# Kernel tuning notes

Hardware: AMD Instinct MI355X
Metric: run time of the kernel (lower is better)

## Reference

```python
import jax, jax.numpy as jnp
import numpy as np

N_NODES = 50000
N_EDGES = 800000
IN_CH = 64
OUT_CH = 64
PRIOR_VAR = 1.0


def setup_inputs() -> dict:
    key = jax.random.key(0)
    ks = jax.random.split(key, 10)
    mean = jax.random.normal(ks[0], (N_NODES, IN_CH), dtype=jnp.float32)
    std = jax.random.uniform(ks[1], (N_NODES, IN_CH), dtype=jnp.float32)
    edge_index = jax.random.randint(ks[2], (2, N_EDGES), 0, N_NODES, dtype=jnp.int32)
    edge_weight = jax.random.uniform(ks[3], (N_EDGES,), dtype=jnp.float32)
    # Bayesian GCN parameters (xavier-ish mu, log_sigma init -3.0) for mean- and std-branches
    scale = float(np.sqrt(6.0 / (IN_CH + OUT_CH)))
    mu_mean = jax.random.uniform(ks[4], (IN_CH, OUT_CH), minval=-scale, maxval=scale, dtype=jnp.float32)
    log_sigma_mean = jnp.full((IN_CH, OUT_CH), -3.0, dtype=jnp.float32)
    mu_std = jax.random.uniform(ks[5], (IN_CH, OUT_CH), minval=-scale, maxval=scale, dtype=jnp.float32)
    log_sigma_std = jnp.full((IN_CH, OUT_CH), -3.0, dtype=jnp.float32)
    # reparameterization noise (drawn once so reference is deterministic)
    eps_mean = jax.random.normal(ks[6], (IN_CH, OUT_CH), dtype=jnp.float32)
    eps_std = jax.random.normal(ks[7], (IN_CH, OUT_CH), dtype=jnp.float32)
    return {
        "mean": mean, "std": std, "edge_index": edge_index, "edge_weight": edge_weight,
        "mu_mean": mu_mean, "log_sigma_mean": log_sigma_mean, "eps_mean": eps_mean,
        "mu_std": mu_std, "log_sigma_std": log_sigma_std, "eps_std": eps_std,
    }


def _gcn_propagate(x, weight, edge_index, edge_weight):
    # support = x @ W; then gather src rows, scale by edge_weight, scatter-add to dst
    support = jnp.matmul(x, weight)                      # [N, out]
    src, dst = edge_index[0], edge_index[1]
    msg = edge_weight[:, None] * support[src]            # [E, out]
    return jax.ops.segment_sum(msg, dst, num_segments=N_NODES)


def _kl(mu, log_sigma):
    pv = PRIOR_VAR
    kl = 0.5 * (jnp.exp(2.0 * log_sigma) / pv + mu ** 2 / pv
                - 2.0 * log_sigma - jnp.log(jnp.asarray(pv, mu.dtype)) - 1.0)
    return kl.sum()


def reference(mean, std, edge_index, edge_weight,
              mu_mean, log_sigma_mean, eps_mean,
              mu_std, log_sigma_std, eps_std):
    # mean branch
    w_mean = mu_mean + eps_mean * jnp.exp(log_sigma_mean)
    new_mean = _gcn_propagate(mean, w_mean, edge_index, edge_weight)
    kl_mean = _kl(mu_mean, log_sigma_mean)
    # std branch operates on variance with squared edge weights
    var = std ** 2
    w_std = mu_std + eps_std * jnp.exp(log_sigma_std)
    new_log_var = _gcn_propagate(var, w_std, edge_index, edge_weight ** 2)
    kl_std = _kl(mu_std, log_sigma_std)
    new_std = jnp.sqrt(jnp.exp(new_log_var) + 1e-6)
    total_kl = kl_mean + kl_std
    return (new_mean, new_std, total_kl)
```

## Files before the change

kernel.cpp:

```cpp
#include <hip/hip_runtime.h>

#define N_NODES 50000
#define N_EDGES 800000
#define CH 64
#define OUT_OFF_STD (N_NODES * CH)
#define OUT_OFF_KL  (2 * N_NODES * CH)
#define CAP 64

#define NGRP 8
#define NPG 6250
#define FILL_CHUNK 2048
#define FILL_CHUNKS 391
#define FILL_BLOCKS (NGRP * FILL_CHUNKS)
#define GEMM_BLOCKS 782
#define GATHER_CHUNKS 1563

typedef __attribute__((ext_vector_type(8))) short short8;
typedef __attribute__((ext_vector_type(4))) float f32x4;

__device__ __forceinline__ int rl_i(unsigned v, int lane) {
    return __builtin_amdgcn_readlane((int)v, lane);
}
__device__ __forceinline__ unsigned f2bf(float f) {
    unsigned u = __float_as_uint(f);
    return (u + 0x7fffu + ((u >> 16) & 1u)) >> 16;
}

__global__ __launch_bounds__(256) void wkl_kernel(
    const float* __restrict__ mu_m, const float* __restrict__ ls_m,
    const float* __restrict__ eps_m,
    const float* __restrict__ mu_s, const float* __restrict__ ls_s,
    const float* __restrict__ eps_s,
    unsigned short* __restrict__ fragBm, unsigned short* __restrict__ fragBv,
    float* __restrict__ kl_out)
{
    __shared__ unsigned short Wm[CH * CH];
    __shared__ unsigned short Wv[CH * CH];
    float kl = 0.0f;
    for (int i = threadIdx.x; i < CH * CH; i += 256) {
        float mu = mu_m[i], ls = ls_m[i];
        Wm[i] = (unsigned short)f2bf(mu + eps_m[i] * expf(ls));
        kl += 0.5f * (expf(2.0f * ls) + mu * mu - 2.0f * ls - 1.0f);
        mu = mu_s[i]; ls = ls_s[i];
        Wv[i] = (unsigned short)f2bf(mu + eps_s[i] * expf(ls));
        kl += 0.5f * (expf(2.0f * ls) + mu * mu - 2.0f * ls - 1.0f);
    }
    __syncthreads();
    for (int f = threadIdx.x; f < CH * CH; f += 256) {
        int j = f & 7, l = (f >> 3) & 63, ch = f >> 9;
        int k = (ch & 1) * 32 + ((l >> 4) & 3) * 8 + j;
        int n = (ch >> 1) * 16 + (l & 15);
        fragBm[f] = Wm[k * CH + n];
        fragBv[f] = Wv[k * CH + n];
    }
    for (int off = 32; off > 0; off >>= 1)
        kl += __shfl_down(kl, off, 64);
    __shared__ float red[4];
    if ((threadIdx.x & 63) == 0) red[threadIdx.x >> 6] = kl;
    __syncthreads();
    if (threadIdx.x == 0)
        kl_out[0] = red[0] + red[1] + red[2] + red[3];
}

__global__ __launch_bounds__(256) void gemfill_kernel(
    const float* __restrict__ mean, const float* __restrict__ stdv,
    const unsigned short* __restrict__ fragBm,
    const unsigned short* __restrict__ fragBv,
    const int* __restrict__ ei, const float* __restrict__ ew,
    int* __restrict__ cur, uint2* __restrict__ bins,
    unsigned* __restrict__ sup)
{
    const int tid = threadIdx.x;

    if (blockIdx.x < FILL_BLOCKS) {
        const int g = blockIdx.x & (NGRP - 1);
        const int chunk = blockIdx.x >> 3;
        const int base = chunk * FILL_CHUNK;
        const int lo = g * NPG;
#pragma unroll
        for (int r = 0; r < FILL_CHUNK / 256; ++r) {
            int e = base + r * 256 + tid;
            if (e < N_EDGES) {
                int dst = ei[N_EDGES + e];
                if ((unsigned)(dst - lo) < (unsigned)NPG) {
                    int src = ei[e];
                    float w = ew[e];
                    int slot = atomicAdd(&cur[dst], 1);
                    if (slot < CAP)
                        bins[(size_t)dst * CAP + slot] =
                            make_uint2((unsigned)src, __float_as_uint(w));
                }
            }
        }
        return;
    }

    const int lane = tid & 63, wave = tid >> 6;
    const int row0 = (blockIdx.x - FILL_BLOCKS) * 64 + wave * 16;
    if (row0 >= N_NODES) return;

    const int m = lane & 15;
    const int q = (lane >> 4) & 3;
    const float* mrow = mean + (size_t)(row0 + m) * CH + q * 8;
    const float* srow = stdv + (size_t)(row0 + m) * CH + q * 8;

    short8 aM[2], aV[2];
#pragma unroll
    for (int h = 0; h < 2; ++h) {
        float4 x0 = *(const float4*)(mrow + h * 32);
        float4 x1 = *(const float4*)(mrow + h * 32 + 4);
        float4 s0 = *(const float4*)(srow + h * 32);
        float4 s1 = *(const float4*)(srow + h * 32 + 4);
        aM[h][0] = (short)f2bf(x0.x); aM[h][1] = (short)f2bf(x0.y);
        aM[h][2] = (short)f2bf(x0.z); aM[h][3] = (short)f2bf(x0.w);
        aM[h][4] = (short)f2bf(x1.x); aM[h][5] = (short)f2bf(x1.y);
        aM[h][6] = (short)f2bf(x1.z); aM[h][7] = (short)f2bf(x1.w);
        aV[h][0] = (short)f2bf(s0.x * s0.x); aV[h][1] = (short)f2bf(s0.y * s0.y);
        aV[h][2] = (short)f2bf(s0.z * s0.z); aV[h][3] = (short)f2bf(s0.w * s0.w);
        aV[h][4] = (short)f2bf(s1.x * s1.x); aV[h][5] = (short)f2bf(s1.y * s1.y);
        aV[h][6] = (short)f2bf(s1.z * s1.z); aV[h][7] = (short)f2bf(s1.w * s1.w);
    }

    f32x4 accM[4], accV[4];
#pragma unroll
    for (int c = 0; c < 4; ++c) {
        accM[c] = (f32x4)0.0f;
        accV[c] = (f32x4)0.0f;
    }
#pragma unroll
    for (int c = 0; c < 4; ++c) {
#pragma unroll
        for (int h = 0; h < 2; ++h) {
            short8 bm = *(const short8*)(fragBm + ((c * 2 + h) * 64 + lane) * 8);
            short8 bv = *(const short8*)(fragBv + ((c * 2 + h) * 64 + lane) * 8);
            accM[c] = __builtin_amdgcn_mfma_f32_16x16x32_bf16(aM[h], bm, accM[c], 0, 0, 0);
            accV[c] = __builtin_amdgcn_mfma_f32_16x16x32_bf16(aV[h], bv, accV[c], 0, 0, 0);
        }
    }

    const int rg = lane >> 4;
#pragma unroll
    for (int c = 0; c < 4; ++c) {
#pragma unroll
        for (int r = 0; r < 4; ++r) {
            int node = row0 + rg * 4 + r;
            sup[(size_t)node * CH + c * 16 + m] =
                f2bf(accM[c][r]) | (f2bf(accV[c][r]) << 16);
        }
    }
}

__global__ __launch_bounds__(256) void gather_kernel(
    const int* __restrict__ cur, const uint2* __restrict__ bins,
    const unsigned* __restrict__ sup, float* __restrict__ out)
{
    const int g = blockIdx.x & (NGRP - 1);
    const int cid = blockIdx.x >> 3;
    const int wave = threadIdx.x >> 6;
    const int col = threadIdx.x & 63;
    const int loc = cid * 4 + wave;
    if (loc >= NPG) return;
    const int n = g * NPG + loc;

    int cnt = cur[n];
    if (cnt > CAP) cnt = CAP;
    uint2 p = make_uint2(0u, 0u);
    if (col < cnt) p = bins[(size_t)n * CAP + col];

    float accM = 0.0f, accV = 0.0f;
    for (int i = 0; i < cnt; i += 8) {
        int   s[8];
        float w[8];
#pragma unroll
        for (int t = 0; t < 8; ++t) {
            bool v = (i + t < cnt);
            s[t] = v ? rl_i(p.x, i + t) : 0;
            w[t] = v ? __uint_as_float((unsigned)rl_i(p.y, i + t)) : 0.0f;
        }
        unsigned q[8];
#pragma unroll
        for (int t = 0; t < 8; ++t)
            q[t] = sup[(size_t)s[t] * CH + col];
#pragma unroll
        for (int t = 0; t < 8; ++t) {
            float mm = __uint_as_float(q[t] << 16);
            float vv = __uint_as_float(q[t] & 0xFFFF0000u);
            accM += w[t] * mm;
            accV += (w[t] * w[t]) * vv;
        }
    }
    out[(size_t)n * CH + col] = accM;
    out[OUT_OFF_STD + (size_t)n * CH + col] = sqrtf(expf(accV) + 1e-6f);
}

extern "C" void kernel_launch(void* const* d_in, const int* in_sizes, int n_in,
                              void* d_out, int out_size, void* d_ws, size_t ws_size,
                              hipStream_t stream)
{
    const float* mean  = (const float*)d_in[0];
    const float* stdv  = (const float*)d_in[1];
    const int*   ei    = (const int*)d_in[2];
    const float* ew    = (const float*)d_in[3];
    const float* mu_m  = (const float*)d_in[4];
    const float* ls_m  = (const float*)d_in[5];
    const float* eps_m = (const float*)d_in[6];
    const float* ls_s  = (const float*)d_in[8];
    const float* mu_s  = (const float*)d_in[7];
    const float* eps_s = (const float*)d_in[9];

    float* out = (float*)d_out;
    int*            cur    = (int*)d_ws;
    unsigned*       sup    = (unsigned*)(cur + N_NODES);
    uint2*          bins   = (uint2*)(sup + (size_t)N_NODES * CH);
    unsigned short* fragBm = (unsigned short*)(bins + (size_t)N_NODES * CAP);
    unsigned short* fragBv = fragBm + CH * CH;

    hipMemsetAsync(cur, 0, N_NODES * sizeof(int), stream);

    wkl_kernel<<<1, 256, 0, stream>>>(mu_m, ls_m, eps_m, mu_s, ls_s, eps_s,
                                      fragBm, fragBv, out + OUT_OFF_KL);
    gemfill_kernel<<<FILL_BLOCKS + GEMM_BLOCKS, 256, 0, stream>>>(
        mean, stdv, fragBm, fragBv, ei, ew, cur, bins, sup);
    gather_kernel<<<NGRP * GATHER_CHUNKS, 256, 0, stream>>>(cur, bins, sup, out);
}
```

Before: 190.3 us.

## Fuse pipeline into one cooperative persistent kernel and pack edge bins to 32 bits

Replaces the memset and three kernel launches with a single cooperative persistent kernel. It zeroes the counters, builds the weights and KL, then splits blocks between the GEMM and edge binning, and runs the gather after grid-wide syncs. Edge bins are packed into one 32-bit word: a 17-bit source index plus a 15-bit fixed-point weight. This halves bin traffic and removes launch gaps, at the cost of lower weight precision, grid.sync overhead and persistent-loop load imbalance. A fallback multi-kernel path remains for when the cooperative launch fails.

```diff
diff --git a/kernel.cpp b/kernel.cpp
--- a/kernel.cpp
+++ b/kernel.cpp
@@ -1,4 +1,7 @@
 #include <hip/hip_runtime.h>
+#include <hip/hip_cooperative_groups.h>
+
+namespace cg = cooperative_groups;
 
 #define N_NODES 50000
 #define N_EDGES 800000
@@ -6,14 +9,11 @@
 #define OUT_OFF_STD (N_NODES * CH)
 #define OUT_OFF_KL  (2 * N_NODES * CH)
 #define CAP 64
-
 #define NGRP 8
 #define NPG 6250
-#define FILL_CHUNK 2048
-#define FILL_CHUNKS 391
-#define FILL_BLOCKS (NGRP * FILL_CHUNKS)
-#define GEMM_BLOCKS 782
-#define GATHER_CHUNKS 1563
+#define GEMM_TILES 782
+#define EDGE_CHUNKS 3125
+#define GQ 1563
 
 typedef __attribute__((ext_vector_type(8))) short short8;
 typedef __attribute__((ext_vector_type(4))) float f32x4;
@@ -25,80 +25,20 @@
     unsigned u = __float_as_uint(f);
     return (u + 0x7fffu + ((u >> 16) & 1u)) >> 16;
 }
-
-__global__ __launch_bounds__(256) void wkl_kernel(
-    const float* __restrict__ mu_m, const float* __restrict__ ls_m,
-    const float* __restrict__ eps_m,
-    const float* __restrict__ mu_s, const float* __restrict__ ls_s,
-    const float* __restrict__ eps_s,
-    unsigned short* __restrict__ fragBm, unsigned short* __restrict__ fragBv,
-    float* __restrict__ kl_out)
-{
-    __shared__ unsigned short Wm[CH * CH];
-    __shared__ unsigned short Wv[CH * CH];
-    float kl = 0.0f;
-    for (int i = threadIdx.x; i < CH * CH; i += 256) {
-        float mu = mu_m[i], ls = ls_m[i];
-        Wm[i] = (unsigned short)f2bf(mu + eps_m[i] * expf(ls));
-        kl += 0.5f * (expf(2.0f * ls) + mu * mu - 2.0f * ls - 1.0f);
-        mu = mu_s[i]; ls = ls_s[i];
-        Wv[i] = (unsigned short)f2bf(mu + eps_s[i] * expf(ls));
-        kl += 0.5f * (expf(2.0f * ls) + mu * mu - 2.0f * ls - 1.0f);
-    }
-    __syncthreads();
-    for (int f = threadIdx.x; f < CH * CH; f += 256) {
-        int j = f & 7, l = (f >> 3) & 63, ch = f >> 9;
-        int k = (ch & 1) * 32 + ((l >> 4) & 3) * 8 + j;
-        int n = (ch >> 1) * 16 + (l & 15);
-        fragBm[f] = Wm[k * CH + n];
-        fragBv[f] = Wv[k * CH + n];
-    }
-    for (int off = 32; off > 0; off >>= 1)
-        kl += __shfl_down(kl, off, 64);
-    __shared__ float red[4];
-    if ((threadIdx.x & 63) == 0) red[threadIdx.x >> 6] = kl;
-    __syncthreads();
-    if (threadIdx.x == 0)
-        kl_out[0] = red[0] + red[1] + red[2] + red[3];
-}
-
-__global__ __launch_bounds__(256) void gemfill_kernel(
+__device__ __forceinline__ unsigned pack_edge(int src, float w) {
+    unsigned wq = (unsigned)(w * 32768.0f + 0.5f);
+    if (wq > 32767u) wq = 32767u;
+    return ((unsigned)src << 15) | wq;
+}
+
+
+__device__ __forceinline__ void gemm_tile(
+    int row0, int lane,
     const float* __restrict__ mean, const float* __restrict__ stdv,
     const unsigned short* __restrict__ fragBm,
     const unsigned short* __restrict__ fragBv,
-    const int* __restrict__ ei, const float* __restrict__ ew,
-    int* __restrict__ cur, uint2* __restrict__ bins,
     unsigned* __restrict__ sup)
 {
-    const int tid = threadIdx.x;
-
-    if (blockIdx.x < FILL_BLOCKS) {
-        const int g = blockIdx.x & (NGRP - 1);
-        const int chunk = blockIdx.x >> 3;
-        const int base = chunk * FILL_CHUNK;
-        const int lo = g * NPG;
-#pragma unroll
-        for (int r = 0; r < FILL_CHUNK / 256; ++r) {
-            int e = base + r * 256 + tid;
-            if (e < N_EDGES) {
-                int dst = ei[N_EDGES + e];
-                if ((unsigned)(dst - lo) < (unsigned)NPG) {
-                    int src = ei[e];
-                    float w = ew[e];
-                    int slot = atomicAdd(&cur[dst], 1);
-                    if (slot < CAP)
-                        bins[(size_t)dst * CAP + slot] =
-                            make_uint2((unsigned)src, __float_as_uint(w));
-                }
-            }
-        }
-        return;
-    }
-
-    const int lane = tid & 63, wave = tid >> 6;
-    const int row0 = (blockIdx.x - FILL_BLOCKS) * 64 + wave * 16;
-    if (row0 >= N_NODES) return;
-
     const int m = lane & 15;
     const int q = (lane >> 4) & 3;
     const float* mrow = mean + (size_t)(row0 + m) * CH + q * 8;
@@ -123,10 +63,7 @@
 
     f32x4 accM[4], accV[4];
 #pragma unroll
-    for (int c = 0; c < 4; ++c) {
-        accM[c] = (f32x4)0.0f;
-        accV[c] = (f32x4)0.0f;
-    }
+    for (int c = 0; c < 4; ++c) { accM[c] = (f32x4)0.0f; accV[c] = (f32x4)0.0f; }
 #pragma unroll
     for (int c = 0; c < 4; ++c) {
 #pragma unroll
@@ -137,60 +74,224 @@
             accV[c] = __builtin_amdgcn_mfma_f32_16x16x32_bf16(aV[h], bv, accV[c], 0, 0, 0);
         }
     }
-
     const int rg = lane >> 4;
 #pragma unroll
-    for (int c = 0; c < 4; ++c) {
+    for (int c = 0; c < 4; ++c)
 #pragma unroll
         for (int r = 0; r < 4; ++r) {
             int node = row0 + rg * 4 + r;
             sup[(size_t)node * CH + c * 16 + m] =
                 f2bf(accM[c][r]) | (f2bf(accV[c][r]) << 16);
         }
-    }
+}
+
+__device__ __forceinline__ void gather_quad(
+    int n, int lane,
+    const int* __restrict__ cur, const unsigned* __restrict__ bins,
+    const unsigned* __restrict__ sup, float* __restrict__ out)
+{
+    int cnt = cur[n];
+    if (cnt > CAP) cnt = CAP;
+    unsigned p = 0u;
+    if (lane < cnt) p = bins[(size_t)n * CAP + lane];
+
+    float accM = 0.0f, accV = 0.0f;
+    for (int i = 0; i < cnt; i += 8) {
+        unsigned u[8];
+#pragma unroll
+        for (int t = 0; t < 8; ++t)
+            u[t] = (i + t < cnt) ? (unsigned)rl_i(p, i + t) : 0u;
+        unsigned q[8];
+#pragma unroll
+        for (int t = 0; t < 8; ++t)
+            q[t] = sup[(size_t)(u[t] >> 15) * CH + lane];
+#pragma unroll
+        for (int t = 0; t < 8; ++t) {
+            float w = (float)(u[t] & 0x7FFFu) * (1.0f / 32768.0f);
+            float mm = __uint_as_float(q[t] << 16);
+            float vv = __uint_as_float(q[t] & 0xFFFF0000u);
+            accM += w * mm;
+            accV += (w * w) * vv;
+        }
+    }
+    out[(size_t)n * CH + lane] = accM;
+    out[OUT_OFF_STD + (size_t)n * CH + lane] = sqrtf(expf(accV) + 1e-6f);
+}
+
+__global__ __launch_bounds__(256) void mono_kernel(
+    const float* __restrict__ mean, const float* __restrict__ stdv,
+    const int* __restrict__ ei, const float* __restrict__ ew,
+    const float* __restrict__ mu_m, const float* __restrict__ ls_m,
+    const float* __restrict__ eps_m,
+    const float* __restrict__ mu_s, const float* __restrict__ ls_s,
+    const float* __restrict__ eps_s,
+    int* __restrict__ cur, unsigned* __restrict__ bins,
+    unsigned* __restrict__ sup,
+    unsigned short* __restrict__ fragBm, unsigned short* __restrict__ fragBv,
+    float* __restrict__ out)
+{
+    cg::grid_group grid = cg::this_grid();
+    const int bid = blockIdx.x;
+    const int tid = threadIdx.x;
+    const int lane = tid & 63, wave = tid >> 6;
+    const int nthreads = gridDim.x * 256;
+
+    __shared__ unsigned short Wm[CH * CH];
+    __shared__ unsigned short Wv[CH * CH];
+    __shared__ float red[4];
+
+    for (int i = bid * 256 + tid; i < N_NODES; i += nthreads)
+        cur[i] = 0;
+    if (bid == 0) {
+        float kl = 0.0f;
+        for (int i = tid; i < CH * CH; i += 256) {
+            float mu = mu_m[i], ls = ls_m[i];
+            Wm[i] = (unsigned short)f2bf(mu + eps_m[i] * expf(ls));
+            kl += 0.5f * (expf(2.0f * ls) + mu * mu - 2.0f * ls - 1.0f);
+            mu = mu_s[i]; ls = ls_s[i];
+            Wv[i] = (unsigned short)f2bf(mu + eps_s[i] * expf(ls));
+            kl += 0.5f * (expf(2.0f * ls) + mu * mu - 2.0f * ls - 1.0f);
+        }
+        __syncthreads();
+        for (int f = tid; f < CH * CH; f += 256) {
+            int j = f & 7, l = (f >> 3) & 63, ch = f >> 9;
+            int k = (ch & 1) * 32 + ((l >> 4) & 3) * 8 + j;
+            int n = (ch >> 1) * 16 + (l & 15);
+            fragBm[f] = Wm[k * CH + n];
+            fragBv[f] = Wv[k * CH + n];
+        }
+        for (int off = 32; off > 0; off >>= 1)
+            kl += __shfl_down(kl, off, 64);
+        if ((tid & 63) == 0) red[tid >> 6] = kl;
+        __syncthreads();
+        if (tid == 0)
+            out[OUT_OFF_KL] = red[0] + red[1] + red[2] + red[3];
+    }
+
+    grid.sync();
+
+    const int G = gridDim.x >> 2;
+    if (bid < G) {
+        for (int t = bid; t < GEMM_TILES; t += G) {
+            int row0 = t * 64 + wave * 16;
+            if (row0 < N_NODES)
+                gemm_tile(row0, lane, mean, stdv, fragBm, fragBv, sup);
+        }
+    } else {
+        const int fb = bid - G;
+        const int F = gridDim.x - G;
+        const int g = fb & (NGRP - 1);
+        const int ci = fb >> 3;
+        const int ng = (F >> 3) + (((F & 7) > g) ? 1 : 0);
+        const int lo = g * NPG;
+        for (int c = ci; c < EDGE_CHUNKS; c += ng) {
+            int e = c * 256 + tid;
+            int dst = ei[N_EDGES + e];
+            if ((unsigned)(dst - lo) < (unsigned)NPG) {
+                int src = ei[e];
+                float w = ew[e];
+                int slot = atomicAdd(&cur[dst], 1);
+                if (slot < CAP)
+                    bins[(size_t)dst * CAP + slot] = pack_edge(src, w);
+            }
+        }
+    }
+
+    grid.sync();
+
+    const int g = bid & (NGRP - 1);
+    const int wg = bid >> 3;
+    const int stride = gridDim.x >> 3;
+    for (int qi = wg; qi < GQ; qi += stride) {
+        const int loc = qi * 4 + wave;
+        if (loc < NPG)
+            gather_quad(g * NPG + loc, lane, cur, bins, sup, out);
+    }
+}
+
+
+__global__ __launch_bounds__(256) void wkl_kernel(
+    const float* __restrict__ mu_m, const float* __restrict__ ls_m,
+    const float* __restrict__ eps_m,
+    const float* __restrict__ mu_s, const float* __restrict__ ls_s,
+    const float* __restrict__ eps_s,
+    unsigned short* __restrict__ fragBm, unsigned short* __restrict__ fragBv,
+    float* __restrict__ kl_out)
+{
+    __shared__ unsigned short Wm[CH * CH];
+    __shared__ unsigned short Wv[CH * CH];
+    float kl = 0.0f;
+    for (int i = threadIdx.x; i < CH * CH; i += 256) {
+        float mu = mu_m[i], ls = ls_m[i];
+        Wm[i] = (unsigned short)f2bf(mu + eps_m[i] * expf(ls));
+        kl += 0.5f * (expf(2.0f * ls) + mu * mu - 2.0f * ls - 1.0f);
+        mu = mu_s[i]; ls = ls_s[i];
+        Wv[i] = (unsigned short)f2bf(mu + eps_s[i] * expf(ls));
+        kl += 0.5f * (expf(2.0f * ls) + mu * mu - 2.0f * ls - 1.0f);
+    }
+    __syncthreads();
+    for (int f = threadIdx.x; f < CH * CH; f += 256) {
+        int j = f & 7, l = (f >> 3) & 63, ch = f >> 9;
+        int k = (ch & 1) * 32 + ((l >> 4) & 3) * 8 + j;
+        int n = (ch >> 1) * 16 + (l & 15);
+        fragBm[f] = Wm[k * CH + n];
+        fragBv[f] = Wv[k * CH + n];
+    }
+    for (int off = 32; off > 0; off >>= 1)
+        kl += __shfl_down(kl, off, 64);
+    __shared__ float red[4];
+    if ((threadIdx.x & 63) == 0) red[threadIdx.x >> 6] = kl;
+    __syncthreads();
+    if (threadIdx.x == 0)
+        kl_out[0] = red[0] + red[1] + red[2] + red[3];
+}
+
+#define FB_FILL_BLOCKS 3128
+__global__ __launch_bounds__(256) void gemfill_kernel(
+    const float* __restrict__ mean, const float* __restrict__ stdv,
+    const unsigned short* __restrict__ fragBm,
+    const unsigned short* __restrict__ fragBv,
+    const int* __restrict__ ei, const float* __restrict__ ew,
+    int* __restrict__ cur, unsigned* __restrict__ bins,
+    unsigned* __restrict__ sup)
+{
+    const int tid = threadIdx.x;
+    if (blockIdx.x < FB_FILL_BLOCKS) {
+        const int g = blockIdx.x & (NGRP - 1);
+        const int chunk = blockIdx.x >> 3;
+        const int base = chunk * 2048;
+        const int lo = g * NPG;
+#pragma unroll
+        for (int r = 0; r < 8; ++r) {
+            int e = base + r * 256 + tid;
+            if (e < N_EDGES) {
+                int dst = ei[N_EDGES + e];
+                if ((unsigned)(dst - lo) < (unsigned)NPG) {
+                    int slot = atomicAdd(&cur[dst], 1);
+                    if (slot < CAP)
+                        bins[(size_t)dst * CAP + slot] = pack_edge(ei[e], ew[e]);
+                }
+            }
+        }
+        return;
+    }
+    const int lane = tid & 63, wave = tid >> 6;
+    const int row0 = (blockIdx.x - FB_FILL_BLOCKS) * 64 + wave * 16;
+    if (row0 >= N_NODES) return;
+    gemm_tile(row0, lane, mean, stdv, fragBm, fragBv, sup);
 }
 
 __global__ __launch_bounds__(256) void gather_kernel(
-    const int* __restrict__ cur, const uint2* __restrict__ bins,
+    const int* __restrict__ cur, const unsigned* __restrict__ bins,
     const unsigned* __restrict__ sup, float* __restrict__ out)
 {
     const int g = blockIdx.x & (NGRP - 1);
     const int cid = blockIdx.x >> 3;
     const int wave = threadIdx.x >> 6;
-    const int col = threadIdx.x & 63;
+    const int lane = threadIdx.x & 63;
     const int loc = cid * 4 + wave;
     if (loc >= NPG) return;
-    const int n = g * NPG + loc;
-
-    int cnt = cur[n];
-    if (cnt > CAP) cnt = CAP;
-    uint2 p = make_uint2(0u, 0u);
-    if (col < cnt) p = bins[(size_t)n * CAP + col];
-
-    float accM = 0.0f, accV = 0.0f;
-    for (int i = 0; i < cnt; i += 8) {
-        int   s[8];
-        float w[8];
-#pragma unroll
-        for (int t = 0; t < 8; ++t) {
-            bool v = (i + t < cnt);
-            s[t] = v ? rl_i(p.x, i + t) : 0;
-            w[t] = v ? __uint_as_float((unsigned)rl_i(p.y, i + t)) : 0.0f;
-        }
-        unsigned q[8];
-#pragma unroll
-        for (int t = 0; t < 8; ++t)
-            q[t] = sup[(size_t)s[t] * CH + col];
-#pragma unroll
-        for (int t = 0; t < 8; ++t) {
-            float mm = __uint_as_float(q[t] << 16);
-            float vv = __uint_as_float(q[t] & 0xFFFF0000u);
-            accM += w[t] * mm;
-            accV += (w[t] * w[t]) * vv;
-        }
-    }
-    out[(size_t)n * CH + col] = accM;
-    out[OUT_OFF_STD + (size_t)n * CH + col] = sqrtf(expf(accV) + 1e-6f);
+    gather_quad(g * NPG + loc, lane, cur, bins, sup, out);
 }
 
 extern "C" void kernel_launch(void* const* d_in, const int* in_sizes, int n_in,
@@ -204,22 +305,45 @@
     const float* mu_m  = (const float*)d_in[4];
     const float* ls_m  = (const float*)d_in[5];
     const float* eps_m = (const float*)d_in[6];
+    const float* mu_s  = (const float*)d_in[7];
     const float* ls_s  = (const float*)d_in[8];
-    const float* mu_s  = (const float*)d_in[7];
     const float* eps_s = (const float*)d_in[9];
 
     float* out = (float*)d_out;
     int*            cur    = (int*)d_ws;
     unsigned*       sup    = (unsigned*)(cur + N_NODES);
-    uint2*          bins   = (uint2*)(sup + (size_t)N_NODES * CH);
+    unsigned*       bins   = (unsigned*)(sup + (size_t)N_NODES * CH);
     unsigned short* fragBm = (unsigned short*)(bins + (size_t)N_NODES * CAP);
     unsigned short* fragBv = fragBm + CH * CH;
 
-    hipMemsetAsync(cur, 0, N_NODES * sizeof(int), stream);
-
-    wkl_kernel<<<1, 256, 0, stream>>>(mu_m, ls_m, eps_m, mu_s, ls_s, eps_s,
-                                      fragBm, fragBv, out + OUT_OFF_KL);
-    gemfill_kernel<<<FILL_BLOCKS + GEMM_BLOCKS, 256, 0, stream>>>(
-        mean, stdv, fragBm, fragBv, ei, ew, cur, bins, sup);
-    gather_kernel<<<NGRP * GATHER_CHUNKS, 256, 0, stream>>>(cur, bins, sup, out);
-}
+    int blocksPerCU = 0;
+    hipError_t qerr = hipOccupancyMaxActiveBlocksPerMultiprocessor(
+        &blocksPerCU, mono_kernel, 256, 0);
+    int grid = 0;
+    if (qerr == hipSuccess && blocksPerCU > 0) {
+        grid = blocksPerCU * 256;
+        if (grid > 2048) grid = 2048;
+        grid &= ~7;
+    }
+
+    hipError_t lerr = hipErrorUnknown;
+    if (grid >= 64) {
+        void* args[] = {
+            (void*)&mean, (void*)&stdv, (void*)&ei, (void*)&ew,
+            (void*)&mu_m, (void*)&ls_m, (void*)&eps_m,
+            (void*)&mu_s, (void*)&ls_s, (void*)&eps_s,
+            (void*)&cur, (void*)&bins, (void*)&sup,
+            (void*)&fragBm, (void*)&fragBv, (void*)&out
+        };
+        lerr = hipLaunchCooperativeKernel((const void*)mono_kernel,
+                                          dim3(grid), dim3(256), args, 0, stream);
+    }
+    if (lerr != hipSuccess) {
+        hipMemsetAsync(cur, 0, N_NODES * sizeof(int), stream);
+        wkl_kernel<<<1, 256, 0, stream>>>(mu_m, ls_m, eps_m, mu_s, ls_s, eps_s,
+                                          fragBm, fragBv, out + OUT_OFF_KL);
+        gemfill_kernel<<<FB_FILL_BLOCKS + GEMM_TILES, 256, 0, stream>>>(
+            mean, stdv, fragBm, fragBv, ei, ew, cur, bins, sup);
+        gather_kernel<<<NGRP * GQ, 256, 0, stream>>>(cur, bins, sup, out);
+    }
+}
```

Result: slower. 363.9 us (+91.3%).
